# Performance work log

Hardware: AMD Instinct MI355X
Metric: run time of the kernel (lower is better)

The kernel has to match this reference:

```python
import jax, jax.numpy as jnp
import numpy as np
import math

D_IN = 1024
D_OUT = 1024
NUM_HEADS = 16
HEAD_DIM = D_OUT // NUM_HEADS
B = 2
S = 4096


def setup_inputs() -> dict:
    key = jax.random.key(0)
    ks = jax.random.split(key, 6)
    x = jax.random.normal(ks[0], (B, S, D_IN), dtype=jnp.float32)
    # kaiming-uniform-ish scale for weights; exact init values don't matter for correctness
    bound = 1.0 / math.sqrt(D_IN)
    Wq = jax.random.uniform(ks[1], (D_OUT, D_IN), minval=-bound, maxval=bound, dtype=jnp.float32)
    Wk = jax.random.uniform(ks[2], (D_OUT, D_IN), minval=-bound, maxval=bound, dtype=jnp.float32)
    Wv = jax.random.uniform(ks[3], (D_OUT, D_IN), minval=-bound, maxval=bound, dtype=jnp.float32)
    Wo = jax.random.uniform(ks[4], (D_OUT, D_OUT), minval=-bound, maxval=bound, dtype=jnp.float32)
    bo = jax.random.uniform(ks[5], (D_OUT,), minval=-bound, maxval=bound, dtype=jnp.float32)
    return {"x": x, "Wq": Wq, "Wk": Wk, "Wv": Wv, "Wo": Wo, "bo": bo}


@jax.custom_vjp
def binarize(w):
    return jnp.sign(w)

def _bin_fwd(w):
    return jnp.sign(w), w

def _bin_bwd(w, g):
    # straight-through estimator: pass grad where |w| <= 1
    return (g * (jnp.abs(w) <= 1).astype(g.dtype),)

binarize.defvjp(_bin_fwd, _bin_bwd)


def reference(x, Wq, Wk, Wv, Wo, bo):
    b, n, _ = x.shape
    h, hd = NUM_HEADS, HEAD_DIM
    # binarized projections (torch F.linear: x @ W.T)
    q = (x @ binarize(Wq).T).reshape(b, n, h, hd).transpose(0, 2, 1, 3)  # [b,h,n,hd]
    k = (x @ binarize(Wk).T).reshape(b, n, h, hd).transpose(0, 2, 1, 3)
    v = (x @ binarize(Wv).T).reshape(b, n, h, hd).transpose(0, 2, 1, 3)
    scores = jnp.einsum('bhqd,bhkd->bhqk', q, k) / math.sqrt(hd)  # [b,h,n,n]
    causal = jnp.tril(jnp.ones((n, n), dtype=bool))
    scores = jnp.where(causal, scores, -jnp.inf)
    attn = jax.nn.softmax(scores, axis=-1)
    # dropout p=0.0 -> identity
    ctx = jnp.einsum('bhqk,bhkd->bqhd', attn, v).reshape(b, n, h * hd)
    return ctx @ binarize(Wo).T + bo
```

## Files before the change

### kernel.cpp

```cpp
#include <hip/hip_runtime.h>
#include <hip/hip_bf16.h>
#include <cstdint>
#include <cstddef>

#define S 4096
#define D 1024
#define H 16
#define HD 64
#define BATCH 2
#define M_TOK 8192
#define K2 2048

typedef short short8 __attribute__((ext_vector_type(8)));
typedef __bf16 bf16x8 __attribute__((ext_vector_type(8)));
typedef float f32x4 __attribute__((ext_vector_type(4)));
typedef unsigned int u32;

static __device__ __forceinline__ ushort f2bf(float f) {
  union { float f; uint32_t u; } v; v.f = f;
  uint32_t u = v.u + 0x7FFFu + ((v.u >> 16) & 1u);
  return (ushort)(u >> 16);
}
static __device__ __forceinline__ float bf2f(ushort h) {
  union { uint32_t u; float f; } v; v.u = ((uint32_t)h) << 16; return v.f;
}
static __device__ __forceinline__ uint32_t cvtpk(float lo, float hi) {
  uint32_t r;
  asm("v_cvt_pk_bf16_f32 %0, %1, %2" : "=v"(r) : "v"(lo), "v"(hi));
  return r;
}
static __device__ __forceinline__ float vexp2(float x) {
  float r;
  asm("v_exp_f32 %0, %1" : "=v"(r) : "v"(x));
  return r;
}
static __device__ __forceinline__ bf16x8 pack4(uint32_t a, uint32_t b, uint32_t c, uint32_t d) {
  union { uint32_t u[4]; bf16x8 v; } z;
  z.u[0] = a; z.u[1] = b; z.u[2] = c; z.u[3] = d;
  return z.v;
}
static __device__ __forceinline__ void gld16(const void* g, void* l) {
  __builtin_amdgcn_global_load_lds(
      (const __attribute__((address_space(1))) u32*)g,
      (__attribute__((address_space(3))) u32*)l, 16, 0, 0);
}
static __device__ __forceinline__ ushort sgn(float a) {
  return a > 0.f ? 0x3F80 : (a < 0.f ? 0xBF80 : 0);
}

__global__ void prep_x(const float* __restrict__ x, ushort* __restrict__ xcat) {
  int i = blockIdx.x * blockDim.x + threadIdx.x;
  const int total = M_TOK * 128;
  for (; i < total; i += gridDim.x * blockDim.x) {
    int row = i >> 7, c8 = (i & 127) * 8;
    const float* px = &x[(size_t)row * 1024 + c8];
    float4 a = *(const float4*)px;
    float4 b = *(const float4*)(px + 4);
    float va[8] = {a.x, a.y, a.z, a.w, b.x, b.y, b.z, b.w};
    union { ushort u[8]; short8 v; } Hh, Ll;
#pragma unroll
    for (int j = 0; j < 8; ++j) {
      ushort h = f2bf(va[j]);
      Hh.u[j] = h;
      Ll.u[j] = f2bf(va[j] - bf2f(h));
    }
    *(short8*)&xcat[(size_t)row * K2 + c8] = Hh.v;
    *(short8*)&xcat[(size_t)row * K2 + 1024 + c8] = Ll.v;
  }
}

__global__ void prep_w(const float* __restrict__ wq, const float* __restrict__ wk,
                       const float* __restrict__ wv, const float* __restrict__ wo,
                       ushort* __restrict__ wcat, ushort* __restrict__ wob) {
  int i = blockIdx.x * blockDim.x + threadIdx.x;
  const int total = (D * D) / 4;
  for (; i < total; i += gridDim.x * blockDim.x) {
    float4 a;
    union { ushort u[4]; uint2 v; } t;
    a = *(const float4*)&wq[i * 4];
    t.u[0] = sgn(a.x); t.u[1] = sgn(a.y); t.u[2] = sgn(a.z); t.u[3] = sgn(a.w);
    *(uint2*)&wcat[i * 4] = t.v;
    a = *(const float4*)&wk[i * 4];
    t.u[0] = sgn(a.x); t.u[1] = sgn(a.y); t.u[2] = sgn(a.z); t.u[3] = sgn(a.w);
    *(uint2*)&wcat[D * D + i * 4] = t.v;
    a = *(const float4*)&wv[i * 4];
    t.u[0] = sgn(a.x); t.u[1] = sgn(a.y); t.u[2] = sgn(a.z); t.u[3] = sgn(a.w);
    *(uint2*)&wcat[2 * D * D + i * 4] = t.v;
    a = *(const float4*)&wo[i * 4];
    t.u[0] = sgn(a.x); t.u[1] = sgn(a.y); t.u[2] = sgn(a.z); t.u[3] = sgn(a.w);
    *(uint2*)&wob[i * 4] = t.v;
  }
}

template<int EPI, int KK, int BROW>
__global__ __launch_bounds__(256) void gemm97(
    const ushort* __restrict__ A, const ushort* __restrict__ Bw,
    ushort* __restrict__ q_hi, ushort* __restrict__ q_lo,
    ushort* __restrict__ k_hi, ushort* __restrict__ k_lo,
    ushort* __restrict__ v_t,
    float* __restrict__ of, const float* __restrict__ bias)
{
  __shared__ ushort smA[128 * 32];
  __shared__ ushort smB[128 * 32];
  const int tid = threadIdx.x;
  const int l = tid & 63;
  const int w = tid >> 6;
  const int x = l & 15, g = l >> 4;
  const int wm = w >> 1, wn = w & 1;
  const int bm = blockIdx.x, bn = blockIdx.y;

  const ushort* gA[2]; const ushort* gB[2]; int ldso[2];
#pragma unroll
  for (int p = 0; p < 2; ++p) {
    int q = p * 256 + tid;
    gA[p] = &A[(size_t)(bm * 128 + (q >> 2)) * KK + (q & 3) * 8];
    gB[p] = &Bw[(size_t)(bn * 128 + (q >> 2)) * BROW + (q & 3) * 8];
    ldso[p] = (p * 256 + w * 64) * 8;
  }

  f32x4 acc[4][4] = {};

  for (int k0 = 0; k0 < KK; k0 += 32) {
    __syncthreads();
#pragma unroll
    for (int p = 0; p < 2; ++p) {
      gld16(gA[p] + k0, &smA[ldso[p]]);
      gld16(gB[p] + (k0 & (BROW - 1)), &smB[ldso[p]]);
    }
    __syncthreads();
    bf16x8 af[4], bf_[4];
#pragma unroll
    for (int m = 0; m < 4; ++m)
      af[m] = *(const bf16x8*)&smA[(wm * 64 + m * 16 + x) * 32 + g * 8];
#pragma unroll
    for (int n = 0; n < 4; ++n)
      bf_[n] = *(const bf16x8*)&smB[(wn * 64 + n * 16 + x) * 32 + g * 8];
#pragma unroll
    for (int m = 0; m < 4; ++m)
#pragma unroll
      for (int n = 0; n < 4; ++n)
        acc[m][n] = __builtin_amdgcn_mfma_f32_16x16x32_bf16(af[m], bf_[n], acc[m][n], 0, 0, 0);
  }

  if (EPI == 0) {
    const int proj = bn >> 3;
    ushort* oh = (proj == 0) ? q_hi : k_hi;
    ushort* ol = (proj == 0) ? q_lo : k_lo;
#pragma unroll
    for (int m = 0; m < 4; ++m)
#pragma unroll
      for (int n = 0; n < 4; ++n)
#pragma unroll
        for (int r = 0; r < 4; ++r) {
          int rowg = bm * 128 + wm * 64 + m * 16 + g * 4 + r;
          int colg = bn * 128 + wn * 64 + n * 16 + x;
          float v = acc[m][n][r];
          int bi = rowg >> 12, ntok = rowg & 4095;
          int cg = colg & 1023;
          int h = cg >> 6, hd = cg & 63;
          size_t bhb = (size_t)(bi * H + h) * (S * HD);
          if (proj < 2) {
            size_t off = bhb + (size_t)ntok * HD + hd;
            ushort hiv = f2bf(v);
            oh[off] = hiv;
            ol[off] = f2bf(v - bf2f(hiv));
          } else {
            int t5 = ntok & 31;
            int pos = ((t5 >> 2) & 3) * 8 + ((t5 >> 4) & 1) * 4 + (t5 & 3);
            v_t[bhb + (size_t)hd * S + (ntok & ~31) + pos] = f2bf(v);
          }
        }
  } else {
#pragma unroll
    for (int m = 0; m < 4; ++m)
#pragma unroll
      for (int n = 0; n < 4; ++n)
#pragma unroll
        for (int r = 0; r < 4; ++r) {
          int rowg = bm * 128 + wm * 64 + m * 16 + g * 4 + r;
          int colg = bn * 128 + wn * 64 + n * 16 + x;
          of[(size_t)rowg * D + colg] = acc[m][n][r] + bias[colg];
        }
  }
}

__global__ __launch_bounds__(512, 2) void flash7(
    const ushort* __restrict__ qhi, const ushort* __restrict__ qlo,
    const ushort* __restrict__ khi, const ushort* __restrict__ klo,
    const ushort* __restrict__ vt, ushort* __restrict__ ctx)
{
  __shared__ ushort smKhi[2][64 * 64];
  __shared__ ushort smKlo[2][64 * 64];
  __shared__ ushort smVT[2][64 * 64];

  const int tid = threadIdx.x;
  const int l = tid & 63;
  const int w = tid >> 6;
  const int wl = w & 3;
  const int x = l & 15;
  const int g = l >> 4;
  const int bh = blockIdx.x;
  const int p = blockIdx.y;
  const int qtw = (w < 4) ? p : (31 - p);
  const int qbase = qtw * 128;
  const size_t qkbase = (size_t)bh * S * HD;

  const int rr = tid >> 3;
  const int sb = (tid & 7) ^ (rr & 7);
  const int soff_k = rr * HD + sb * 8;
  const size_t soff_v = (size_t)rr * S + sb * 8;
  const int ldso = w * 512;

  const ushort* khb = khi + qkbase;
  const ushort* klb = klo + qkbase;
  const ushort* vtb = vt + qkbase;

  bf16x8 bq[2][2][2];
#pragma unroll
  for (int qs = 0; qs < 2; ++qs) {
    int qrow = qbase + wl * 32 + qs * 16 + x;
    size_t base = qkbase + (size_t)qrow * HD + g * 8;
    bq[qs][0][0] = *(const bf16x8*)&qhi[base];
    bq[qs][0][1] = *(const bf16x8*)&qhi[base + 32];
    bq[qs][1][0] = *(const bf16x8*)&qlo[base];
    bq[qs][1][1] = *(const bf16x8*)&qlo[base + 32];
  }

  float mrun[2] = {-1e30f, -1e30f};
  float lrun[2] = {0.f, 0.f};
  f32x4 oacc[2][4] = {};

  const int kvmax = 2 * (31 - p) + 1;
  const int qmaxw = qbase + wl * 32 + 31;
  const float C1 = 0.125f * 1.44269504f;
  const float TH = 8.0f / C1;

  gld16(khb + soff_k, &smKhi[0][ldso]);
  gld16(klb + soff_k, &smKlo[0][ldso]);
  gld16(vtb + soff_v, &smVT[0][ldso]);
  __syncthreads();

  int cur = 0;
  for (int kv = 0; kv <= kvmax; ++kv) {
    if (kv < kvmax) {
      const ushort* kh = khb + (size_t)(kv + 1) * (64 * HD);
      const ushort* kl = klb + (size_t)(kv + 1) * (64 * HD);
      const ushort* vp = vtb + (size_t)(kv + 1) * 64;
      int nb = cur ^ 1;
      gld16(kh + soff_k, &smKhi[nb][ldso]);
      gld16(kl + soff_k, &smKlo[nb][ldso]);
      gld16(vp + soff_v, &smVT[nb][ldso]);
    }

    if (kv * 64 <= qmaxw) {
      const ushort* bKhi = smKhi[cur];
      const ushort* bKlo = smKlo[cur];
      const ushort* bVT = smVT[cur];

      f32x4 scq[2][4];
      __builtin_amdgcn_s_setprio(1);
#pragma unroll
      for (int t = 0; t < 4; ++t) {
        f32x4 a0 = {}, a1 = {};
#pragma unroll
        for (int c = 0; c < 2; ++c) {
          int pb = (t * 16 + x) * 64 + ((4 * c + g) ^ (x & 7)) * 8;
          bf16x8 kH = *(const bf16x8*)&bKhi[pb];
          bf16x8 kL = *(const bf16x8*)&bKlo[pb];
          a0 = __builtin_amdgcn_mfma_f32_16x16x32_bf16(kH, bq[0][0][c], a0, 0, 0, 0);
          a0 = __builtin_amdgcn_mfma_f32_16x16x32_bf16(kL, bq[0][0][c], a0, 0, 0, 0);
          a0 = __builtin_amdgcn_mfma_f32_16x16x32_bf16(kH, bq[0][1][c], a0, 0, 0, 0);
          a1 = __builtin_amdgcn_mfma_f32_16x16x32_bf16(kH, bq[1][0][c], a1, 0, 0, 0);
          a1 = __builtin_amdgcn_mfma_f32_16x16x32_bf16(kL, bq[1][0][c], a1, 0, 0, 0);
          a1 = __builtin_amdgcn_mfma_f32_16x16x32_bf16(kH, bq[1][1][c], a1, 0, 0, 0);
        }
        scq[0][t] = a0; scq[1][t] = a1;
      }
      __builtin_amdgcn_s_setprio(0);

      const bool needmask = (kv * 64 + 63 > qbase + wl * 32);
      uint32_t pbq[2][2][4];

#pragma unroll
      for (int qs = 0; qs < 2; ++qs) {
        if (needmask) {
          int qglob = qbase + wl * 32 + qs * 16 + x;
          int kb = kv * 64 + 4 * g;
#pragma unroll
          for (int t = 0; t < 4; ++t)
#pragma unroll
            for (int r = 0; r < 4; ++r)
              if (kb + t * 16 + r > qglob) scq[qs][t][r] = -1e30f;
        }
        float mt[4];
#pragma unroll
        for (int t = 0; t < 4; ++t)
          mt[t] = fmaxf(fmaxf(scq[qs][t][0], scq[qs][t][1]),
                        fmaxf(scq[qs][t][2], scq[qs][t][3]));
        float mloc = fmaxf(fmaxf(mt[0], mt[1]), fmaxf(mt[2], mt[3]));
        if (__any(mloc > mrun[qs] + TH)) {
          mloc = fmaxf(mloc, __shfl_xor(mloc, 16));
          mloc = fmaxf(mloc, __shfl_xor(mloc, 32));
          float mnew = fmaxf(mrun[qs], mloc);
          float scal = vexp2((mrun[qs] - mnew) * C1);
          mrun[qs] = mnew;
          lrun[qs] *= scal;
#pragma unroll
          for (int dt = 0; dt < 4; ++dt) oacc[qs][dt] *= scal;
        }
        float mc = mrun[qs] * C1;
#pragma unroll
        for (int t = 0; t < 4; ++t)
#pragma unroll
          for (int r = 0; r < 4; ++r)
            scq[qs][t][r] = vexp2(scq[qs][t][r] * C1 - mc);
        float st[4];
#pragma unroll
        for (int t = 0; t < 4; ++t)
          st[t] = (scq[qs][t][0] + scq[qs][t][1]) + (scq[qs][t][2] + scq[qs][t][3]);
        lrun[qs] += (st[0] + st[1]) + (st[2] + st[3]);
#pragma unroll
        for (int c = 0; c < 2; ++c) {
          pbq[qs][c][0] = cvtpk(scq[qs][2 * c][0], scq[qs][2 * c][1]);
          pbq[qs][c][1] = cvtpk(scq[qs][2 * c][2], scq[qs][2 * c][3]);
          pbq[qs][c][2] = cvtpk(scq[qs][2 * c + 1][0], scq[qs][2 * c + 1][1]);
          pbq[qs][c][3] = cvtpk(scq[qs][2 * c + 1][2], scq[qs][2 * c + 1][3]);
        }
      }

      __builtin_amdgcn_s_setprio(1);
#pragma unroll
      for (int c = 0; c < 2; ++c)
#pragma unroll
        for (int dt = 0; dt < 4; ++dt) {
          bf16x8 vf = *(const bf16x8*)&bVT[(dt * 16 + x) * 64 + ((4 * c + g) ^ (x & 7)) * 8];
          oacc[0][dt] = __builtin_amdgcn_mfma_f32_16x16x32_bf16(
              vf, pack4(pbq[0][c][0], pbq[0][c][1], pbq[0][c][2], pbq[0][c][3]), oacc[0][dt], 0, 0, 0);
          oacc[1][dt] = __builtin_amdgcn_mfma_f32_16x16x32_bf16(
              vf, pack4(pbq[1][c][0], pbq[1][c][1], pbq[1][c][2], pbq[1][c][3]), oacc[1][dt], 0, 0, 0);
        }
      __builtin_amdgcn_s_setprio(0);
    }

    __syncthreads();
    cur ^= 1;
  }

  const int b = bh >> 4, h = bh & 15;
#pragma unroll
  for (int qs = 0; qs < 2; ++qs) {
    float ls = lrun[qs];
    ls += __shfl_xor(ls, 16);
    ls += __shfl_xor(ls, 32);
    float inv = 1.0f / ls;
    int tok = qbase + wl * 32 + qs * 16 + x;
#pragma unroll
    for (int dt = 0; dt < 4; ++dt) {
      uint2 uu;
      uu.x = cvtpk(oacc[qs][dt][0] * inv, oacc[qs][dt][1] * inv);
      uu.y = cvtpk(oacc[qs][dt][2] * inv, oacc[qs][dt][3] * inv);
      *(uint2*)&ctx[(size_t)(b * S + tok) * D + h * 64 + dt * 16 + 4 * g] = uu;
    }
  }
}

extern "C" void kernel_launch(void* const* d_in, const int* in_sizes, int n_in,
                              void* d_out, int out_size, void* d_ws, size_t ws_size,
                              hipStream_t stream) {
  const float* x  = (const float*)d_in[0];
  const float* Wq = (const float*)d_in[1];
  const float* Wk = (const float*)d_in[2];
  const float* Wv = (const float*)d_in[3];
  const float* Wo = (const float*)d_in[4];
  const float* bo = (const float*)d_in[5];
  float* out = (float*)d_out;

  if (ws_size < (size_t)120 * 1024 * 1024) return;

  char* ws = (char*)d_ws;
  const size_t MB = 1024 * 1024;
  ushort* xcat = (ushort*)(ws);
  ushort* ctx  = (ushort*)(ws);
  ushort* wcat = (ushort*)(ws + 32 * MB);
  ushort* wob  = (ushort*)(ws + 38 * MB);
  ushort* qhi  = (ushort*)(ws + 40 * MB);
  ushort* qlo  = (ushort*)(ws + 56 * MB);
  ushort* khi  = (ushort*)(ws + 72 * MB);
  ushort* klo  = (ushort*)(ws + 88 * MB);
  ushort* vt   = (ushort*)(ws + 104 * MB);

  prep_x<<<2048, 256, 0, stream>>>(x, xcat);
  prep_w<<<1024, 256, 0, stream>>>(Wq, Wk, Wv, Wo, wcat, wob);

  gemm97<0, K2, 1024><<<dim3(64, 24), 256, 0, stream>>>(
      xcat, wcat, qhi, qlo, khi, klo, vt, nullptr, nullptr);

  flash7<<<dim3(BATCH * H, 16), 512, 0, stream>>>(qhi, qlo, khi, klo, vt, ctx);

  gemm97<2, 1024, 1024><<<dim3(64, 8), 256, 0, stream>>>(
      ctx, wob, nullptr, nullptr, nullptr, nullptr, nullptr, out, bo);
}
```

Before: 364.1 us.

## Drop LDS staging in flash attention; load K/V fragments directly from global

```diff
diff --git a/kernel.cpp b/kernel.cpp
--- a/kernel.cpp
+++ b/kernel.cpp
@@ -184,78 +184,65 @@
   }
 }
 
-__global__ __launch_bounds__(512, 2) void flash7(
+__global__ __launch_bounds__(256) void flash8(
     const ushort* __restrict__ qhi, const ushort* __restrict__ qlo,
     const ushort* __restrict__ khi, const ushort* __restrict__ klo,
     const ushort* __restrict__ vt, ushort* __restrict__ ctx)
 {
-  __shared__ ushort smKhi[2][64 * 64];
-  __shared__ ushort smKlo[2][64 * 64];
-  __shared__ ushort smVT[2][64 * 64];
-
   const int tid = threadIdx.x;
   const int l = tid & 63;
-  const int w = tid >> 6;
-  const int wl = w & 3;
+  const int wl = tid >> 6;
   const int x = l & 15;
   const int g = l >> 4;
   const int bh = blockIdx.x;
   const int p = blockIdx.y;
-  const int qtw = (w < 4) ? p : (31 - p);
-  const int qbase = qtw * 128;
   const size_t qkbase = (size_t)bh * S * HD;
-
-  const int rr = tid >> 3;
-  const int sb = (tid & 7) ^ (rr & 7);
-  const int soff_k = rr * HD + sb * 8;
-  const size_t soff_v = (size_t)rr * S + sb * 8;
-  const int ldso = w * 512;
 
   const ushort* khb = khi + qkbase;
   const ushort* klb = klo + qkbase;
   const ushort* vtb = vt + qkbase;
-
-  bf16x8 bq[2][2][2];
-#pragma unroll
-  for (int qs = 0; qs < 2; ++qs) {
-    int qrow = qbase + wl * 32 + qs * 16 + x;
-    size_t base = qkbase + (size_t)qrow * HD + g * 8;
-    bq[qs][0][0] = *(const bf16x8*)&qhi[base];
-    bq[qs][0][1] = *(const bf16x8*)&qhi[base + 32];
-    bq[qs][1][0] = *(const bf16x8*)&qlo[base];
-    bq[qs][1][1] = *(const bf16x8*)&qlo[base + 32];
-  }
-
-  float mrun[2] = {-1e30f, -1e30f};
-  float lrun[2] = {0.f, 0.f};
-  f32x4 oacc[2][4] = {};
-
-  const int kvmax = 2 * (31 - p) + 1;
-  const int qmaxw = qbase + wl * 32 + 31;
+  const int b = bh >> 4, h = bh & 15;
+
   const float C1 = 0.125f * 1.44269504f;
   const float TH = 8.0f / C1;
 
-  gld16(khb + soff_k, &smKhi[0][ldso]);
-  gld16(klb + soff_k, &smKlo[0][ldso]);
-  gld16(vtb + soff_v, &smVT[0][ldso]);
-  __syncthreads();
-
-  int cur = 0;
-  for (int kv = 0; kv <= kvmax; ++kv) {
-    if (kv < kvmax) {
-      const ushort* kh = khb + (size_t)(kv + 1) * (64 * HD);
-      const ushort* kl = klb + (size_t)(kv + 1) * (64 * HD);
-      const ushort* vp = vtb + (size_t)(kv + 1) * 64;
-      int nb = cur ^ 1;
-      gld16(kh + soff_k, &smKhi[nb][ldso]);
-      gld16(kl + soff_k, &smKlo[nb][ldso]);
-      gld16(vp + soff_v, &smVT[nb][ldso]);
-    }
-
-    if (kv * 64 <= qmaxw) {
-      const ushort* bKhi = smKhi[cur];
-      const ushort* bKlo = smKlo[cur];
-      const ushort* bVT = smVT[cur];
+  for (int half = 0; half < 2; ++half) {
+    const int qtw = half ? (31 - p) : p;
+    const int qbase = qtw * 128;
+
+    bf16x8 bq[2][2][2];
+#pragma unroll
+    for (int qs = 0; qs < 2; ++qs) {
+      int qrow = qbase + wl * 32 + qs * 16 + x;
+      size_t base = qkbase + (size_t)qrow * HD + g * 8;
+      bq[qs][0][0] = *(const bf16x8*)&qhi[base];
+      bq[qs][0][1] = *(const bf16x8*)&qhi[base + 32];
+      bq[qs][1][0] = *(const bf16x8*)&qlo[base];
+      bq[qs][1][1] = *(const bf16x8*)&qlo[base + 32];
+    }
+
+    float mrun[2] = {-1e30f, -1e30f};
+    float lrun[2] = {0.f, 0.f};
+    f32x4 oacc[2][4] = {};
+
+    const int kvmax = (qbase + wl * 32 + 31) >> 6;
+
+    const ushort* kpl = khb + x * HD + g * 8;
+    const ushort* klpl = klb + x * HD + g * 8;
+    const ushort* vpl = vtb + (size_t)x * S + g * 8;
+
+    for (int kv = 0; kv <= kvmax; ++kv) {
+      const ushort* kp = kpl + (size_t)kv * (64 * HD);
+      const ushort* klp = klpl + (size_t)kv * (64 * HD);
+
+      bf16x8 kH[4][2], kL[4][2];
+#pragma unroll
+      for (int t = 0; t < 4; ++t)
+#pragma unroll
+        for (int c = 0; c < 2; ++c) {
+          kH[t][c] = *(const bf16x8*)&kp[t * 16 * HD + c * 32];
+          kL[t][c] = *(const bf16x8*)&klp[t * 16 * HD + c * 32];
+        }
 
       f32x4 scq[2][4];
       __builtin_amdgcn_s_setprio(1);
@@ -264,19 +251,23 @@
         f32x4 a0 = {}, a1 = {};
 #pragma unroll
         for (int c = 0; c < 2; ++c) {
-          int pb = (t * 16 + x) * 64 + ((4 * c + g) ^ (x & 7)) * 8;
-          bf16x8 kH = *(const bf16x8*)&bKhi[pb];
-          bf16x8 kL = *(const bf16x8*)&bKlo[pb];
-          a0 = __builtin_amdgcn_mfma_f32_16x16x32_bf16(kH, bq[0][0][c], a0, 0, 0, 0);
-          a0 = __builtin_amdgcn_mfma_f32_16x16x32_bf16(kL, bq[0][0][c], a0, 0, 0, 0);
-          a0 = __builtin_amdgcn_mfma_f32_16x16x32_bf16(kH, bq[0][1][c], a0, 0, 0, 0);
-          a1 = __builtin_amdgcn_mfma_f32_16x16x32_bf16(kH, bq[1][0][c], a1, 0, 0, 0);
-          a1 = __builtin_amdgcn_mfma_f32_16x16x32_bf16(kL, bq[1][0][c], a1, 0, 0, 0);
-          a1 = __builtin_amdgcn_mfma_f32_16x16x32_bf16(kH, bq[1][1][c], a1, 0, 0, 0);
+          a0 = __builtin_amdgcn_mfma_f32_16x16x32_bf16(kH[t][c], bq[0][0][c], a0, 0, 0, 0);
+          a0 = __builtin_amdgcn_mfma_f32_16x16x32_bf16(kL[t][c], bq[0][0][c], a0, 0, 0, 0);
+          a0 = __builtin_amdgcn_mfma_f32_16x16x32_bf16(kH[t][c], bq[0][1][c], a0, 0, 0, 0);
+          a1 = __builtin_amdgcn_mfma_f32_16x16x32_bf16(kH[t][c], bq[1][0][c], a1, 0, 0, 0);
+          a1 = __builtin_amdgcn_mfma_f32_16x16x32_bf16(kL[t][c], bq[1][0][c], a1, 0, 0, 0);
+          a1 = __builtin_amdgcn_mfma_f32_16x16x32_bf16(kH[t][c], bq[1][1][c], a1, 0, 0, 0);
         }
         scq[0][t] = a0; scq[1][t] = a1;
       }
       __builtin_amdgcn_s_setprio(0);
+
+      bf16x8 vv[2][4];
+#pragma unroll
+      for (int c = 0; c < 2; ++c)
+#pragma unroll
+        for (int dt = 0; dt < 4; ++dt)
+          vv[c][dt] = *(const bf16x8*)&vpl[(size_t)(dt * 16) * S + kv * 64 + c * 32];
 
       const bool needmask = (kv * 64 + 63 > qbase + wl * 32);
       uint32_t pbq[2][2][4];
@@ -333,33 +324,28 @@
       for (int c = 0; c < 2; ++c)
 #pragma unroll
         for (int dt = 0; dt < 4; ++dt) {
-          bf16x8 vf = *(const bf16x8*)&bVT[(dt * 16 + x) * 64 + ((4 * c + g) ^ (x & 7)) * 8];
           oacc[0][dt] = __builtin_amdgcn_mfma_f32_16x16x32_bf16(
-              vf, pack4(pbq[0][c][0], pbq[0][c][1], pbq[0][c][2], pbq[0][c][3]), oacc[0][dt], 0, 0, 0);
+              vv[c][dt], pack4(pbq[0][c][0], pbq[0][c][1], pbq[0][c][2], pbq[0][c][3]), oacc[0][dt], 0, 0, 0);
           oacc[1][dt] = __builtin_amdgcn_mfma_f32_16x16x32_bf16(
-              vf, pack4(pbq[1][c][0], pbq[1][c][1], pbq[1][c][2], pbq[1][c][3]), oacc[1][dt], 0, 0, 0);
+              vv[c][dt], pack4(pbq[1][c][0], pbq[1][c][1], pbq[1][c][2], pbq[1][c][3]), oacc[1][dt], 0, 0, 0);
         }
       __builtin_amdgcn_s_setprio(0);
     }
 
-    __syncthreads();
-    cur ^= 1;
-  }
-
-  const int b = bh >> 4, h = bh & 15;
-#pragma unroll
-  for (int qs = 0; qs < 2; ++qs) {
-    float ls = lrun[qs];
-    ls += __shfl_xor(ls, 16);
-    ls += __shfl_xor(ls, 32);
-    float inv = 1.0f / ls;
-    int tok = qbase + wl * 32 + qs * 16 + x;
-#pragma unroll
-    for (int dt = 0; dt < 4; ++dt) {
-      uint2 uu;
-      uu.x = cvtpk(oacc[qs][dt][0] * inv, oacc[qs][dt][1] * inv);
-      uu.y = cvtpk(oacc[qs][dt][2] * inv, oacc[qs][dt][3] * inv);
-      *(uint2*)&ctx[(size_t)(b * S + tok) * D + h * 64 + dt * 16 + 4 * g] = uu;
+#pragma unroll
+    for (int qs = 0; qs < 2; ++qs) {
+      float ls = lrun[qs];
+      ls += __shfl_xor(ls, 16);
+      ls += __shfl_xor(ls, 32);
+      float inv = 1.0f / ls;
+      int tok = qbase + wl * 32 + qs * 16 + x;
+#pragma unroll
+      for (int dt = 0; dt < 4; ++dt) {
+        uint2 uu;
+        uu.x = cvtpk(oacc[qs][dt][0] * inv, oacc[qs][dt][1] * inv);
+        uu.y = cvtpk(oacc[qs][dt][2] * inv, oacc[qs][dt][3] * inv);
+        *(uint2*)&ctx[(size_t)(b * S + tok) * D + h * 64 + dt * 16 + 4 * g] = uu;
+      }
     }
   }
 }
@@ -395,7 +381,7 @@
   gemm97<0, K2, 1024><<<dim3(64, 24), 256, 0, stream>>>(
       xcat, wcat, qhi, qlo, khi, klo, vt, nullptr, nullptr);
 
-  flash7<<<dim3(BATCH * H, 16), 512, 0, stream>>>(qhi, qlo, khi, klo, vt, ctx);
+  flash8<<<dim3(BATCH * H, 16), 256, 0, stream>>>(qhi, qlo, khi, klo, vt, ctx);
 
   gemm97<2, 1024, 1024><<<dim3(64, 8), 256, 0, stream>>>(
       ctx, wob, nullptr, nullptr, nullptr, nullptr, nullptr, out, bo);
```

After: 520.7 us. 43.0% more time.
